# Optimization experiments

Hardware: AMD Instinct MI355X
Metric: run time of the kernel (lower is better)

The kernel has to match this reference:

```python
import math
import jax, jax.numpy as jnp
import numpy as np

B, T, D = 1, 4096, 1024
NH, NKV, HD = 16, 4, 64          # nhead, n_kv_heads, head_dim
WINDOW = 256


def _alibi_slopes(nhead: int) -> np.ndarray:
    closest_pow2 = 2 ** math.floor(math.log2(nhead))
    base = 2.0 ** (-2.0 ** (-(math.log2(closest_pow2) - 3)))
    slopes = base ** np.arange(1, closest_pow2 + 1, dtype=np.float32)
    if closest_pow2 < nhead:
        extra_base = 2.0 ** (-2.0 ** (-(math.log2(2 * closest_pow2) - 3)))
        extra = extra_base ** np.arange(1, 2 * (nhead - closest_pow2) + 1, 2, dtype=np.float32)
        slopes = np.concatenate([slopes, extra])
    return slopes.astype(np.float32)


def setup_inputs() -> dict:
    key = jax.random.key(0)
    ks = jax.random.split(key, 9)
    s = 0.02
    return {
        "x": jax.random.normal(ks[0], (B, T, D), jnp.float32),
        "Wq": jax.random.normal(ks[1], (D, NH * HD), jnp.float32) * s,
        "bq": jax.random.normal(ks[2], (NH * HD,), jnp.float32) * s,
        "Wk": jax.random.normal(ks[3], (D, NKV * HD), jnp.float32) * s,
        "bk": jax.random.normal(ks[4], (NKV * HD,), jnp.float32) * s,
        "Wv": jax.random.normal(ks[5], (D, NKV * HD), jnp.float32) * s,
        "bv": jax.random.normal(ks[6], (NKV * HD,), jnp.float32) * s,
        "Wo": jax.random.normal(ks[7], (D, D), jnp.float32) * s,
        "bo": jax.random.normal(ks[8], (D,), jnp.float32) * s,
    }


def _attn_bias():
    # ALiBi bias + causal + sliding-window mask, shape (NH, T, T)
    pos = jnp.arange(T)
    dist = pos[None, :] - pos[:, None]          # col - row; <=0 where causal-allowed
    allowed = (dist <= 0) & (-dist < WINDOW)    # causal AND within window
    slopes = jnp.asarray(_alibi_slopes(NH))     # (NH,)
    bias = -slopes[:, None, None] * jnp.abs(dist)[None].astype(jnp.float32)
    return jnp.where(allowed[None], bias, -jnp.inf)  # (NH, T, T)


def reference(x, Wq, bq, Wk, bk, Wv, bv, Wo, bo):
    q = (x @ Wq + bq).reshape(B, T, NH, HD).transpose(0, 2, 1, 3)   # (B,NH,T,HD)
    k = (x @ Wk + bk).reshape(B, T, NKV, HD).transpose(0, 2, 1, 3)  # (B,NKV,T,HD)
    v = (x @ Wv + bv).reshape(B, T, NKV, HD).transpose(0, 2, 1, 3)
    # GQA: repeat_interleave kv heads to NH
    k = jnp.repeat(k, NH // NKV, axis=1)
    v = jnp.repeat(v, NH // NKV, axis=1)
    scale = 1.0 / math.sqrt(HD)
    scores = jnp.einsum("bhtd,bhsd->bhts", q, k) * scale + _attn_bias()[None]
    probs = jax.nn.softmax(scores, axis=-1)
    out = jnp.einsum("bhts,bhsd->bhtd", probs, v)        # (B,NH,T,HD)
    out = out.transpose(0, 2, 1, 3).reshape(B, T, D)
    return out @ Wo + bo
```

## Files before the change

kernel.cpp:

```cpp
#include <hip/hip_runtime.h>

typedef __bf16 bf16;
typedef __bf16 bf16x8 __attribute__((ext_vector_type(8)));
typedef float f32x4 __attribute__((ext_vector_type(4)));

#define T_LEN   4096
#define D_MODEL 1024
#define QKV_LD  1536
#define VT_LD   4128
#define WINDOW  256

__device__ __forceinline__ void gload_lds16(const bf16* g, bf16* l) {
    __builtin_amdgcn_global_load_lds((const __attribute__((address_space(1))) void*)g,
                                     (__attribute__((address_space(3))) void*)l, 16, 0, 0);
}


__global__ void cvt_f32_bf16(const float* __restrict__ in, bf16* __restrict__ out, int n) {
    int i = (blockIdx.x * blockDim.x + threadIdx.x) * 8;
    if (i >= n) return;
    float4 a = *(const float4*)(in + i);
    float4 b = *(const float4*)(in + i + 4);
    bf16x8 o;
    o[0] = (bf16)a.x; o[1] = (bf16)a.y; o[2] = (bf16)a.z; o[3] = (bf16)a.w;
    o[4] = (bf16)b.x; o[5] = (bf16)b.y; o[6] = (bf16)b.z; o[7] = (bf16)b.w;
    *(bf16x8*)(out + i) = o;
}

__global__ void concat_bias(const float* __restrict__ bq, const float* __restrict__ bk,
                            const float* __restrict__ bv, float* __restrict__ out) {
    int i = blockIdx.x * blockDim.x + threadIdx.x;
    if (i < 1024)      out[i] = bq[i];
    else if (i < 1280) out[i] = bk[i - 1024];
    else               out[i] = bv[i - 1280];
}

__global__ void transpose_wqkv(const float* __restrict__ Wq, const float* __restrict__ Wk,
                               const float* __restrict__ Wv, bf16* __restrict__ Wt) {
    __shared__ float t[32][33];
    int n0 = blockIdx.x * 32, k0 = blockIdx.y * 32;
    const float* W; int Ns, nofs;
    if (n0 < 1024)      { W = Wq; Ns = 1024; nofs = 0; }
    else if (n0 < 1280) { W = Wk; Ns = 256;  nofs = 1024; }
    else                { W = Wv; Ns = 256;  nofs = 1280; }
    int tx = threadIdx.x & 31, ty = threadIdx.x >> 5;
#pragma unroll
    for (int it = 0; it < 4; ++it)
        t[ty + it * 8][tx] = W[(size_t)(k0 + ty + it * 8) * Ns + (n0 - nofs) + tx];
    __syncthreads();
#pragma unroll
    for (int it = 0; it < 4; ++it)
        Wt[(size_t)(n0 + ty + it * 8) * 1024 + k0 + tx] = (bf16)t[tx][ty + it * 8];
}

__global__ void transpose_w(const float* __restrict__ W, bf16* __restrict__ Wt, int K, int N) {
    __shared__ float t[32][33];
    int n0 = blockIdx.x * 32, k0 = blockIdx.y * 32;
    int tx = threadIdx.x & 31, ty = threadIdx.x >> 5;
#pragma unroll
    for (int it = 0; it < 4; ++it)
        t[ty + it * 8][tx] = W[(size_t)(k0 + ty + it * 8) * N + n0 + tx];
    __syncthreads();
#pragma unroll
    for (int it = 0; it < 4; ++it)
        Wt[(size_t)(n0 + ty + it * 8) * K + k0 + tx] = (bf16)t[tx][ty + it * 8];
}

__global__ void transpose_v(const bf16* __restrict__ QKV, bf16* __restrict__ Vt) {
    __shared__ bf16 t[32][33];
    int t0 = blockIdx.x * 32;
    int c0 = blockIdx.y * 32;
    int tx = threadIdx.x & 31, ty = threadIdx.x >> 5;
#pragma unroll
    for (int it = 0; it < 4; ++it)
        t[ty + it * 8][tx] = QKV[(size_t)(t0 + ty + it * 8) * QKV_LD + 1280 + c0 + tx];
    __syncthreads();
#pragma unroll
    for (int it = 0; it < 4; ++it)
        Vt[(size_t)(c0 + ty + it * 8) * VT_LD + t0 + tx] = t[tx][ty + it * 8];
}


template <bool OUT_BF16>
__global__ __launch_bounds__(256) void gemm_bt(
    const bf16* __restrict__ A, const bf16* __restrict__ Bt,
    const float* __restrict__ bias, void* __restrict__ Cv,
    int M, int N, int K)
{
    __shared__ bf16 As[128 * 32];
    __shared__ bf16 Bs[128 * 32];
    const int m0 = blockIdx.y * 128;
    const int n0 = blockIdx.x * 128;
    const int tid  = threadIdx.x;
    const int wave = tid >> 6, lane = tid & 63;
    const int quad = lane >> 4, l16 = lane & 15;
    const int wm = wave >> 1, wn = wave & 1;

    f32x4 acc[4][4] = {};

    const int srow = wave * 32 + (lane >> 2);
    const int scol = (lane & 3) * 8;
    const bf16* ga0 = A  + (size_t)(m0 + srow) * K + scol;
    const bf16* ga1 = A  + (size_t)(m0 + srow + 16) * K + scol;
    const bf16* gb0 = Bt + (size_t)(n0 + srow) * K + scol;
    const bf16* gb1 = Bt + (size_t)(n0 + srow + 16) * K + scol;
    bf16* la0 = As + srow * 32 + scol;
    bf16* la1 = As + (srow + 16) * 32 + scol;
    bf16* lb0 = Bs + srow * 32 + scol;
    bf16* lb1 = Bs + (srow + 16) * 32 + scol;

    const int nk = K >> 5;
    for (int kt = 0; kt < nk; ++kt) {
        __syncthreads();
        gload_lds16(ga0 + kt * 32, la0);
        gload_lds16(ga1 + kt * 32, la1);
        gload_lds16(gb0 + kt * 32, lb0);
        gload_lds16(gb1 + kt * 32, lb1);
        __syncthreads();
        bf16x8 af[4], bfr[4];
#pragma unroll
        for (int i = 0; i < 4; ++i)
            af[i] = *(const bf16x8*)&As[(wm * 64 + i * 16 + l16) * 32 + quad * 8];
#pragma unroll
        for (int j = 0; j < 4; ++j)
            bfr[j] = *(const bf16x8*)&Bs[(wn * 64 + j * 16 + l16) * 32 + quad * 8];
#pragma unroll
        for (int i = 0; i < 4; ++i)
#pragma unroll
            for (int j = 0; j < 4; ++j)
                acc[i][j] = __builtin_amdgcn_mfma_f32_16x16x32_bf16(af[i], bfr[j], acc[i][j], 0, 0, 0);
    }

#pragma unroll
    for (int i = 0; i < 4; ++i)
#pragma unroll
        for (int j = 0; j < 4; ++j) {
            const int col = n0 + wn * 64 + j * 16 + l16;
            const float bb = bias[col];
#pragma unroll
            for (int r = 0; r < 4; ++r) {
                const int row = m0 + wm * 64 + i * 16 + quad * 4 + r;
                const float v = acc[i][j][r] + bb;
                if (OUT_BF16) ((bf16*)Cv)[(size_t)row * N + col] = (bf16)v;
                else          ((float*)Cv)[(size_t)row * N + col] = v;
            }
        }
}


__global__ __launch_bounds__(64) void attn_kernel(
    const bf16* __restrict__ QKV, const bf16* __restrict__ Vt, bf16* __restrict__ Oa)
{
    __shared__ bf16 Ps[16][296];
    const int q0 = blockIdx.x * 16;
    const int h  = blockIdx.y;
    const int kh = h >> 2;
    const int lane = threadIdx.x;
    const int quad = lane >> 4, l16 = lane & 15;
    const float slope = exp2f(-0.5f * (float)(h + 1));
    const int lo = (q0 >= 256) ? (q0 - 256) : 0;

    const bf16* qp = QKV + (size_t)(q0 + l16) * QKV_LD + h * 64 + quad * 8;
    bf16x8 qf0 = *(const bf16x8*)qp;
    bf16x8 qf1 = *(const bf16x8*)(qp + 32);

    f32x4 s[17];
#pragma unroll
    for (int t = 0; t < 17; ++t) {
        const bf16* kp = QKV + (size_t)(lo + t * 16 + l16) * QKV_LD + D_MODEL + kh * 64 + quad * 8;
        bf16x8 kf0 = *(const bf16x8*)kp;
        bf16x8 kf1 = *(const bf16x8*)(kp + 32);
        f32x4 a = {};
        a = __builtin_amdgcn_mfma_f32_16x16x32_bf16(qf0, kf0, a, 0, 0, 0);
        a = __builtin_amdgcn_mfma_f32_16x16x32_bf16(qf1, kf1, a, 0, 0, 0);
        s[t] = a;
    }

    float rinv[4];
#pragma unroll
    for (int r = 0; r < 4; ++r) {
        const int row = q0 + quad * 4 + r;
        float mx = -1e30f;
#pragma unroll
        for (int t = 0; t < 17; ++t) {
            const int key = lo + t * 16 + l16;
            float v = s[t][r] * 0.125f - slope * (float)(row - key);
            const bool ok = (key <= row) && (key > row - WINDOW);
            v = ok ? v : -1e30f;
            s[t][r] = v;
            mx = fmaxf(mx, v);
        }
#pragma unroll
        for (int d = 1; d < 16; d <<= 1) mx = fmaxf(mx, __shfl_xor(mx, d));
        float sum = 0.f;
#pragma unroll
        for (int t = 0; t < 17; ++t) {
            float p = __expf(s[t][r] - mx);
            s[t][r] = p;
            sum += p;
        }
#pragma unroll
        for (int d = 1; d < 16; d <<= 1) sum += __shfl_xor(sum, d);
        rinv[r] = 1.f / sum;
    }

    {
        int idx = lane;
#pragma unroll
        for (int it = 0; it < 4; ++it) {
            Ps[(idx >> 4) & 15][272 + (idx & 15)] = (bf16)0.f;
            idx += 64;
        }
    }
#pragma unroll
    for (int t = 0; t < 17; ++t)
#pragma unroll
        for (int r = 0; r < 4; ++r)
            Ps[quad * 4 + r][t * 16 + l16] = (bf16)(s[t][r] * rinv[r]);
    __syncthreads();

    f32x4 o[4] = {};
#pragma unroll
    for (int c = 0; c < 9; ++c) {
        bf16x8 pf = *(const bf16x8*)&Ps[l16][c * 32 + quad * 8];
#pragma unroll
        for (int j = 0; j < 4; ++j) {
            const bf16* vp = Vt + (size_t)(kh * 64 + j * 16 + l16) * VT_LD + lo + c * 32 + quad * 8;
            bf16x8 vf = *(const bf16x8*)vp;
            o[j] = __builtin_amdgcn_mfma_f32_16x16x32_bf16(pf, vf, o[j], 0, 0, 0);
        }
    }

#pragma unroll
    for (int j = 0; j < 4; ++j)
#pragma unroll
        for (int r = 0; r < 4; ++r)
            Oa[(size_t)(q0 + quad * 4 + r) * D_MODEL + h * 64 + j * 16 + l16] = (bf16)o[j][r];
}


extern "C" void kernel_launch(void* const* d_in, const int* in_sizes, int n_in,
                              void* d_out, int out_size, void* d_ws, size_t ws_size,
                              hipStream_t stream) {
    const float* x  = (const float*)d_in[0];
    const float* Wq = (const float*)d_in[1];
    const float* bq = (const float*)d_in[2];
    const float* Wk = (const float*)d_in[3];
    const float* bk = (const float*)d_in[4];
    const float* Wv = (const float*)d_in[5];
    const float* bv = (const float*)d_in[6];
    const float* Wo = (const float*)d_in[7];
    const float* bo = (const float*)d_in[8];
    float* out = (float*)d_out;

    char* ws = (char*)d_ws;
    bf16*  xb    = (bf16*)(ws);
    bf16*  WtQKV = (bf16*)(ws + 8388608);
    bf16*  WtO   = (bf16*)(ws + 11534336);
    float* biasQ = (float*)(ws + 13631488);
    bf16*  QKV   = (bf16*)(ws + 13637632);
    bf16*  Vt    = (bf16*)(ws + 26220544);
    bf16*  AO    = (bf16*)(ws + 28334080);

    cvt_f32_bf16<<<2048, 256, 0, stream>>>(x, xb, 4096 * 1024);
    concat_bias<<<6, 256, 0, stream>>>(bq, bk, bv, biasQ);
    transpose_wqkv<<<dim3(48, 32), 256, 0, stream>>>(Wq, Wk, Wv, WtQKV);
    transpose_w<<<dim3(32, 32), 256, 0, stream>>>(Wo, WtO, 1024, 1024);

    gemm_bt<true><<<dim3(12, 32), 256, 0, stream>>>(xb, WtQKV, biasQ, QKV, 4096, 1536, 1024);
    transpose_v<<<dim3(128, 8), 256, 0, stream>>>(QKV, Vt);
    attn_kernel<<<dim3(256, 16), 64, 0, stream>>>(QKV, Vt, AO);
    gemm_bt<false><<<dim3(8, 32), 256, 0, stream>>>(AO, WtO, bo, out, 4096, 1024, 1024);
}
```

Baseline: 188.5 us.

## Shrink GEMM N-tile, pack four attention waves per block, fuse bias concat

The GEMM tile shrinks from 128x128 to 128x64, doubling the block count for the QKV and output projections so more of the GPU's compute units are filled. The attention kernel now runs four independent 16-query waves per 256-thread block, with a separate LDS slice per wave, instead of one wave per block. The concat_bias launch is removed and the QKV GEMM epilogue picks the bias from bq, bk or bv directly. The smaller GEMM tile lowers data reuse per block, and the larger attention LDS footprint may reduce how many blocks fit per CU.

```diff
diff --git a/kernel.cpp b/kernel.cpp
--- a/kernel.cpp
+++ b/kernel.cpp
@@ -27,14 +27,6 @@
     *(bf16x8*)(out + i) = o;
 }
 
-__global__ void concat_bias(const float* __restrict__ bq, const float* __restrict__ bk,
-                            const float* __restrict__ bv, float* __restrict__ out) {
-    int i = blockIdx.x * blockDim.x + threadIdx.x;
-    if (i < 1024)      out[i] = bq[i];
-    else if (i < 1280) out[i] = bk[i - 1024];
-    else               out[i] = bv[i - 1280];
-}
-
 __global__ void transpose_wqkv(const float* __restrict__ Wq, const float* __restrict__ Wk,
                                const float* __restrict__ Wv, bf16* __restrict__ Wt) {
     __shared__ float t[32][33];
@@ -81,62 +73,62 @@
 }
 
 
-template <bool OUT_BF16>
+template <bool OUT_BF16, bool QKV_BIAS>
 __global__ __launch_bounds__(256) void gemm_bt(
     const bf16* __restrict__ A, const bf16* __restrict__ Bt,
-    const float* __restrict__ bias, void* __restrict__ Cv,
+    const float* __restrict__ b0, const float* __restrict__ b1,
+    const float* __restrict__ b2, void* __restrict__ Cv,
     int M, int N, int K)
 {
     __shared__ bf16 As[128 * 32];
-    __shared__ bf16 Bs[128 * 32];
+    __shared__ bf16 Bs[64 * 32];
     const int m0 = blockIdx.y * 128;
-    const int n0 = blockIdx.x * 128;
+    const int n0 = blockIdx.x * 64;
     const int tid  = threadIdx.x;
     const int wave = tid >> 6, lane = tid & 63;
     const int quad = lane >> 4, l16 = lane & 15;
     const int wm = wave >> 1, wn = wave & 1;
 
-    f32x4 acc[4][4] = {};
-
-    const int srow = wave * 32 + (lane >> 2);
+    f32x4 acc[4][2] = {};
+
+    const int srow = wave * 16 + (lane >> 2);
     const int scol = (lane & 3) * 8;
     const bf16* ga0 = A  + (size_t)(m0 + srow) * K + scol;
-    const bf16* ga1 = A  + (size_t)(m0 + srow + 16) * K + scol;
-    const bf16* gb0 = Bt + (size_t)(n0 + srow) * K + scol;
-    const bf16* gb1 = Bt + (size_t)(n0 + srow + 16) * K + scol;
+    const bf16* ga1 = A  + (size_t)(m0 + srow + 64) * K + scol;
+    const bf16* gb  = Bt + (size_t)(n0 + srow) * K + scol;
     bf16* la0 = As + srow * 32 + scol;
-    bf16* la1 = As + (srow + 16) * 32 + scol;
-    bf16* lb0 = Bs + srow * 32 + scol;
-    bf16* lb1 = Bs + (srow + 16) * 32 + scol;
+    bf16* la1 = As + (srow + 64) * 32 + scol;
+    bf16* lb  = Bs + srow * 32 + scol;
 
     const int nk = K >> 5;
     for (int kt = 0; kt < nk; ++kt) {
         __syncthreads();
         gload_lds16(ga0 + kt * 32, la0);
         gload_lds16(ga1 + kt * 32, la1);
-        gload_lds16(gb0 + kt * 32, lb0);
-        gload_lds16(gb1 + kt * 32, lb1);
+        gload_lds16(gb  + kt * 32, lb);
         __syncthreads();
-        bf16x8 af[4], bfr[4];
+        bf16x8 af[4], bfr[2];
 #pragma unroll
         for (int i = 0; i < 4; ++i)
             af[i] = *(const bf16x8*)&As[(wm * 64 + i * 16 + l16) * 32 + quad * 8];
 #pragma unroll
-        for (int j = 0; j < 4; ++j)
-            bfr[j] = *(const bf16x8*)&Bs[(wn * 64 + j * 16 + l16) * 32 + quad * 8];
+        for (int j = 0; j < 2; ++j)
+            bfr[j] = *(const bf16x8*)&Bs[(wn * 32 + j * 16 + l16) * 32 + quad * 8];
 #pragma unroll
         for (int i = 0; i < 4; ++i)
 #pragma unroll
-            for (int j = 0; j < 4; ++j)
+            for (int j = 0; j < 2; ++j)
                 acc[i][j] = __builtin_amdgcn_mfma_f32_16x16x32_bf16(af[i], bfr[j], acc[i][j], 0, 0, 0);
     }
 
 #pragma unroll
     for (int i = 0; i < 4; ++i)
 #pragma unroll
-        for (int j = 0; j < 4; ++j) {
-            const int col = n0 + wn * 64 + j * 16 + l16;
-            const float bb = bias[col];
+        for (int j = 0; j < 2; ++j) {
+            const int col = n0 + wn * 32 + j * 16 + l16;
+            const float bb = QKV_BIAS
+                ? (col < 1024 ? b0[col] : (col < 1280 ? b1[col - 1024] : b2[col - 1280]))
+                : b0[col];
 #pragma unroll
             for (int r = 0; r < 4; ++r) {
                 const int row = m0 + wm * 64 + i * 16 + quad * 4 + r;
@@ -148,14 +140,15 @@
 }
 
 
-__global__ __launch_bounds__(64) void attn_kernel(
+__global__ __launch_bounds__(256) void attn_kernel(
     const bf16* __restrict__ QKV, const bf16* __restrict__ Vt, bf16* __restrict__ Oa)
 {
-    __shared__ bf16 Ps[16][296];
-    const int q0 = blockIdx.x * 16;
+    __shared__ bf16 Ps[4][16][296];
+    const int wave = threadIdx.x >> 6;
+    const int lane = threadIdx.x & 63;
+    const int q0 = (blockIdx.x * 4 + wave) * 16;
     const int h  = blockIdx.y;
     const int kh = h >> 2;
-    const int lane = threadIdx.x;
     const int quad = lane >> 4, l16 = lane & 15;
     const float slope = exp2f(-0.5f * (float)(h + 1));
     const int lo = (q0 >= 256) ? (q0 - 256) : 0;
@@ -208,7 +201,7 @@
         int idx = lane;
 #pragma unroll
         for (int it = 0; it < 4; ++it) {
-            Ps[(idx >> 4) & 15][272 + (idx & 15)] = (bf16)0.f;
+            Ps[wave][(idx >> 4) & 15][272 + (idx & 15)] = (bf16)0.f;
             idx += 64;
         }
     }
@@ -216,13 +209,13 @@
     for (int t = 0; t < 17; ++t)
 #pragma unroll
         for (int r = 0; r < 4; ++r)
-            Ps[quad * 4 + r][t * 16 + l16] = (bf16)(s[t][r] * rinv[r]);
+            Ps[wave][quad * 4 + r][t * 16 + l16] = (bf16)(s[t][r] * rinv[r]);
     __syncthreads();
 
     f32x4 o[4] = {};
 #pragma unroll
     for (int c = 0; c < 9; ++c) {
-        bf16x8 pf = *(const bf16x8*)&Ps[l16][c * 32 + quad * 8];
+        bf16x8 pf = *(const bf16x8*)&Ps[wave][l16][c * 32 + quad * 8];
 #pragma unroll
         for (int j = 0; j < 4; ++j) {
             const bf16* vp = Vt + (size_t)(kh * 64 + j * 16 + l16) * VT_LD + lo + c * 32 + quad * 8;
@@ -257,18 +250,16 @@
     bf16*  xb    = (bf16*)(ws);
     bf16*  WtQKV = (bf16*)(ws + 8388608);
     bf16*  WtO   = (bf16*)(ws + 11534336);
-    float* biasQ = (float*)(ws + 13631488);
     bf16*  QKV   = (bf16*)(ws + 13637632);
     bf16*  Vt    = (bf16*)(ws + 26220544);
     bf16*  AO    = (bf16*)(ws + 28334080);
 
     cvt_f32_bf16<<<2048, 256, 0, stream>>>(x, xb, 4096 * 1024);
-    concat_bias<<<6, 256, 0, stream>>>(bq, bk, bv, biasQ);
     transpose_wqkv<<<dim3(48, 32), 256, 0, stream>>>(Wq, Wk, Wv, WtQKV);
     transpose_w<<<dim3(32, 32), 256, 0, stream>>>(Wo, WtO, 1024, 1024);
 
-    gemm_bt<true><<<dim3(12, 32), 256, 0, stream>>>(xb, WtQKV, biasQ, QKV, 4096, 1536, 1024);
+    gemm_bt<true, true><<<dim3(24, 32), 256, 0, stream>>>(xb, WtQKV, bq, bk, bv, QKV, 4096, 1536, 1024);
     transpose_v<<<dim3(128, 8), 256, 0, stream>>>(QKV, Vt);
-    attn_kernel<<<dim3(256, 16), 64, 0, stream>>>(QKV, Vt, AO);
-    gemm_bt<false><<<dim3(8, 32), 256, 0, stream>>>(AO, WtO, bo, out, 4096, 1024, 1024);
-}
+    attn_kernel<<<dim3(64, 16), 256, 0, stream>>>(QKV, Vt, AO);
+    gemm_bt<false, false><<<dim3(16, 32), 256, 0, stream>>>(AO, WtO, bo, nullptr, nullptr, out, 4096, 1024, 1024);
+}
```

Measured after the change: 181.2 us. -3.8%, faster.
